# Kernel optimization log

Measured on AMD Instinct MI355X. Metric: run time of the kernel, lower is better.

The kernel has to match this reference:

```python
import jax, jax.numpy as jnp
import numpy as np
import math

DIM_MODEL = 1024
N_HEAD = 16
NUM_NEURON = 64
MAX_LEN = 2048
B, S = 4, 2048


def setup_inputs() -> dict:
    key = jax.random.key(0)
    ks = jax.random.split(key, 11)
    d, p = DIM_MODEL, N_HEAD * NUM_NEURON
    sc_in = 1.0 / math.sqrt(d)
    sc_p = 1.0 / math.sqrt(p)
    return {
        "q": jax.random.normal(ks[0], (B, S, d), jnp.float32),
        "k": jax.random.normal(ks[1], (B, S, d), jnp.float32),
        "v": jax.random.normal(ks[2], (B, S, d), jnp.float32),
        "Wq": jax.random.normal(ks[3], (d, p), jnp.float32) * sc_in,
        "bq": jnp.zeros((p,), jnp.float32),
        "Wk": jax.random.normal(ks[4], (d, p), jnp.float32) * sc_in,
        "bk": jnp.zeros((p,), jnp.float32),
        "Wv": jax.random.normal(ks[5], (d, p), jnp.float32) * sc_in,
        "bv": jnp.zeros((p,), jnp.float32),
        "Wf": jax.random.normal(ks[6], (p, d), jnp.float32) * sc_p,
        "bf": jnp.zeros((d,), jnp.float32),
    }


def _split_heads(x):  # [B,S,H*Dh] -> [B,H,S,Dh]
    b, s, _ = x.shape
    return x.reshape(b, s, N_HEAD, NUM_NEURON).transpose(0, 2, 1, 3)


def reference(q, k, v, Wq, bq, Wk, bk, Wv, bv, Wf, bf):
    qh = _split_heads(q @ Wq + bq)
    kh = _split_heads(k @ Wk + bk)
    vh = _split_heads(v @ Wv + bv)
    # NOTE: original scales by 1/sqrt(max_len), not 1/sqrt(head_dim)
    scores = jnp.einsum("bhqd,bhkd->bhqk", qh, kh) / math.sqrt(MAX_LEN)
    s = scores.shape[-1]
    causal = jnp.tril(jnp.ones((s, s), bool))  # [S,S]
    scores = jnp.where(causal[None, None], scores, -jnp.inf)
    attn = jax.nn.softmax(scores, axis=-1)
    out = jnp.einsum("bhqk,bhkd->bhqd", attn, vh)  # [B,H,S,Dh]
    c = out.transpose(0, 2, 1, 3).reshape(out.shape[0], out.shape[2], N_HEAD * NUM_NEURON)
    return c @ Wf + bf
```

## Files before the change

### kernel.cpp

```cpp
#include <hip/hip_runtime.h>
#include <stdint.h>

#define DMODEL 1024
#define NHEAD 16
#define DH 64
#define BB 4
#define SS 2048
#define MROWS (BB * SS)

typedef __bf16 bfx8 __attribute__((ext_vector_type(8)));
typedef float f32x4 __attribute__((ext_vector_type(4)));
typedef float fvec4 __attribute__((ext_vector_type(4)));
typedef int i32x4 __attribute__((ext_vector_type(4)));
typedef unsigned short u16x8 __attribute__((ext_vector_type(8)));
typedef unsigned short u16x4 __attribute__((ext_vector_type(4)));

__device__ __forceinline__ unsigned short f2bf(float f) {
    union { float f; unsigned int u; } v; v.f = f;
    unsigned int r = v.u + 0x7FFFu + ((v.u >> 16) & 1u);
    return (unsigned short)(r >> 16);
}

__device__ __forceinline__ unsigned int cvtpk(float lo, float hi) {
    unsigned int r;
    asm("v_cvt_pk_bf16_f32 %0, %1, %2" : "=v"(r) : "v"(lo), "v"(hi));
    return r;
}

typedef __attribute__((address_space(1))) const void gas_t;
typedef __attribute__((address_space(3))) void las_t;
__device__ __forceinline__ void gload_lds16(const void* g, void* l) {
    __builtin_amdgcn_global_load_lds((gas_t*)g, (las_t*)l, 16, 0, 0);
}

__device__ __forceinline__ int sigma_k(int i) {
    return (i & 0x20) | ((i & 0x0C) << 1) | ((i & 0x10) >> 2) | (i & 3);
}

__global__ void cvt3_kernel(const float* __restrict__ s0, const float* __restrict__ s1,
                            const float* __restrict__ s2,
                            unsigned short* __restrict__ d0, unsigned short* __restrict__ d1,
                            unsigned short* __restrict__ d2, int n8)
{
    const float* s = (blockIdx.y == 0) ? s0 : (blockIdx.y == 1) ? s1 : s2;
    unsigned short* d = (blockIdx.y == 0) ? d0 : (blockIdx.y == 1) ? d1 : d2;
    int i = blockIdx.x * blockDim.x + threadIdx.x;
    if (i >= n8) return;
    fvec4 a = *reinterpret_cast<const fvec4*>(&s[(size_t)i * 8]);
    fvec4 b = *reinterpret_cast<const fvec4*>(&s[(size_t)i * 8 + 4]);
    u16x8 o;
    #pragma unroll
    for (int j = 0; j < 4; ++j) { o[j] = f2bf(a[j]); o[j + 4] = f2bf(b[j]); }
    *reinterpret_cast<u16x8*>(&d[(size_t)i * 8]) = o;
}

__global__ void transpose_cvt3_kernel(const float* __restrict__ W0, unsigned short* __restrict__ T0,
                                      const float* __restrict__ W1, unsigned short* __restrict__ T1,
                                      const float* __restrict__ W2, unsigned short* __restrict__ T2)
{
    const float* W = (blockIdx.z == 0) ? W0 : (blockIdx.z == 1) ? W1 : W2;
    unsigned short* Wt = (blockIdx.z == 0) ? T0 : (blockIdx.z == 1) ? T1 : T2;
    __shared__ unsigned short t[64][72];
    const int tid = threadIdx.x;
    const int r0 = blockIdx.y * 64, c0 = blockIdx.x * 64;
    #pragma unroll
    for (int i = 0; i < 4; ++i) {
        int idx = tid + i * 256;
        int r = idx >> 4, c4 = idx & 15;
        fvec4 v = *reinterpret_cast<const fvec4*>(&W[(size_t)(r0 + r) * DMODEL + c0 + c4 * 4]);
        #pragma unroll
        for (int j = 0; j < 4; ++j) t[c4 * 4 + j][r] = f2bf(v[j]);
    }
    __syncthreads();
    #pragma unroll
    for (int i = 0; i < 2; ++i) {
        int idx = tid + i * 256;
        int r = idx >> 3, c8 = idx & 7;
        u16x8 v = *reinterpret_cast<const u16x8*>(&t[r][c8 * 8]);
        *reinterpret_cast<u16x8*>(&Wt[(size_t)(c0 + r) * DMODEL + r0 + c8 * 8]) = v;
    }
}

__global__ void transpose_v_kernel(const unsigned short* __restrict__ Vb,
                                   unsigned short* __restrict__ Vt)
{
    __shared__ unsigned short t[64][72];
    const int tid = threadIdx.x;
    const int s0 = blockIdx.x * 64, bh = blockIdx.y;
    const int b = bh >> 4, h = bh & 15;
    #pragma unroll
    for (int i = 0; i < 2; ++i) {
        int idx = tid + i * 256;
        int sr = idx >> 3, c8 = idx & 7;
        u16x8 v = *reinterpret_cast<const u16x8*>(
            &Vb[((size_t)b * SS + s0 + sr) * DMODEL + h * DH + c8 * 8]);
        #pragma unroll
        for (int j = 0; j < 8; ++j) t[c8 * 8 + j][sr] = v[j];
    }
    __syncthreads();
    #pragma unroll
    for (int i = 0; i < 2; ++i) {
        int idx = tid + i * 256;
        int dr = idx >> 3, s8 = idx & 7;
        u16x8 v = *reinterpret_cast<const u16x8*>(&t[dr][s8 * 8]);
        *reinterpret_cast<u16x8*>(&Vt[((size_t)bh * DH + dr) * SS + s0 + s8 * 8]) = v;
    }
}

struct GArg {
    const unsigned short* A;
    const unsigned short* Bt;
    const float* bias;
    void* O;
    float osc;
};

template<bool OUT_BF16>
__global__ __launch_bounds__(256, 2)
void gemm_kernel(GArg g0, GArg g1, int M, int N, int K)
{
    const GArg g = blockIdx.z ? g1 : g0;
    __shared__ unsigned short sA[128 * 64];
    __shared__ unsigned short sB[128 * 64];
    const int tid  = threadIdx.x;
    const int lane = tid & 63;
    const int wave = tid >> 6;
    const int wm = (wave >> 1) * 64, wn = (wave & 1) * 64;
    const int m0 = blockIdx.x * 128, n0 = blockIdx.y * 128;
    const int lr = lane & 15;
    const int lg = lane >> 4;

    f32x4 acc[4][4] = {};

    for (int kk0 = 0; kk0 < K; kk0 += 64) {
        __syncthreads();
        #pragma unroll
        for (int i = 0; i < 4; ++i) {
            int c = tid + i * 256;
            int row = c >> 3, col8 = c & 7;
            gload_lds16(&g.A[(size_t)(m0 + row) * K + kk0 + col8 * 8], &sA[c * 8]);
        }
        #pragma unroll
        for (int i = 0; i < 4; ++i) {
            int c = tid + i * 256;
            int row = c >> 3, col8 = c & 7;
            gload_lds16(&g.Bt[(size_t)(n0 + row) * K + kk0 + col8 * 8], &sB[c * 8]);
        }
        __syncthreads();

        bfx8 af[4][2], bfr[4][2];
        #pragma unroll
        for (int m = 0; m < 4; ++m)
            #pragma unroll
            for (int kk = 0; kk < 2; ++kk)
                af[m][kk] = *reinterpret_cast<const bfx8*>(
                    &sA[(wm + m * 16 + lr) * 64 + kk * 32 + lg * 8]);
        #pragma unroll
        for (int n = 0; n < 4; ++n)
            #pragma unroll
            for (int kk = 0; kk < 2; ++kk)
                bfr[n][kk] = *reinterpret_cast<const bfx8*>(
                    &sB[(wn + n * 16 + lr) * 64 + kk * 32 + lg * 8]);
        #pragma unroll
        for (int kk = 0; kk < 2; ++kk)
            #pragma unroll
            for (int m = 0; m < 4; ++m)
                #pragma unroll
                for (int n = 0; n < 4; ++n)
                    acc[m][n] = __builtin_amdgcn_mfma_f32_16x16x32_bf16(
                        af[m][kk], bfr[n][kk], acc[m][n], 0, 0, 0);
    }

    #pragma unroll
    for (int n = 0; n < 4; ++n) {
        int col = n0 + wn + n * 16 + lr;
        float bv = g.bias[col];
        #pragma unroll
        for (int m = 0; m < 4; ++m) {
            int rowb = m0 + wm + m * 16 + lg * 4;
            #pragma unroll
            for (int r = 0; r < 4; ++r) {
                float val = (acc[m][n][r] + bv) * g.osc;
                if (OUT_BF16)
                    ((unsigned short*)g.O)[(size_t)(rowb + r) * N + col] = f2bf(val);
                else
                    ((float*)g.O)[(size_t)(rowb + r) * N + col] = val;
            }
        }
    }
}

__global__ __launch_bounds__(256, 2)
void attn_kernel(const unsigned short* __restrict__ Q,
                 const unsigned short* __restrict__ K,
                 const unsigned short* __restrict__ Vt,
                 unsigned short* __restrict__ C)
{
    __shared__ unsigned short sK[64][72];
    __shared__ unsigned short sVt[64][72];

    const int tid  = threadIdx.x;
    const int lane = tid & 63;
    const int wave = tid >> 6;
    const int lr = lane & 15, lg = lane >> 4;
    const int bh = blockIdx.x;
    const int qt = (int)(gridDim.y - 1) - (int)blockIdx.y;
    const int b = bh >> 4, h = bh & 15;
    const int q0 = qt * 128;
    const size_t rowbase = (size_t)b * SS;
    const int hcol = h * DH;

    const int srow = tid >> 3, sc8 = tid & 7;
    const int sig0 = sigma_k(srow), sig1 = sigma_k(srow + 32);

    bfx8 aq[2][2];
    #pragma unroll
    for (int m = 0; m < 2; ++m) {
        int qr = q0 + wave * 32 + m * 16 + lr;
        const unsigned short* p = &Q[(rowbase + qr) * DMODEL + hcol + lg * 8];
        aq[m][0] = *reinterpret_cast<const bfx8*>(p);
        aq[m][1] = *reinterpret_cast<const bfx8*>(p + 32);
    }

    float m_run[2] = {0.f, 0.f};
    f32x4 l4[2] = {};
    f32x4 acc_o[2][4] = {};
    bool mz = true;
    const int qmax_wave = q0 + wave * 32 + 31;
    const int ntiles = 2 * qt + 2;

    for (int t = 0; t < ntiles; ++t) {
        const int k0 = t * 64;
        __syncthreads();
        *reinterpret_cast<u16x8*>(&sK[srow][sc8 * 8]) =
            *reinterpret_cast<const u16x8*>(
                &K[(rowbase + k0 + sig0) * DMODEL + hcol + sc8 * 8]);
        *reinterpret_cast<u16x8*>(&sK[srow + 32][sc8 * 8]) =
            *reinterpret_cast<const u16x8*>(
                &K[(rowbase + k0 + sig1) * DMODEL + hcol + sc8 * 8]);
        *reinterpret_cast<u16x8*>(&sVt[srow][sc8 * 8]) =
            *reinterpret_cast<const u16x8*>(
                &Vt[((size_t)bh * DH + srow) * SS + k0 + sc8 * 8]);
        *reinterpret_cast<u16x8*>(&sVt[srow + 32][sc8 * 8]) =
            *reinterpret_cast<const u16x8*>(
                &Vt[((size_t)bh * DH + srow + 32) * SS + k0 + sc8 * 8]);
        __syncthreads();
        if (k0 > qmax_wave) continue;

        f32x4 sc[2][4];
        #pragma unroll
        for (int nf = 0; nf < 4; ++nf) {
            bfx8 ak0 = *reinterpret_cast<const bfx8*>(&sK[nf * 16 + lr][lg * 8]);
            bfx8 ak1 = *reinterpret_cast<const bfx8*>(&sK[nf * 16 + lr][32 + lg * 8]);
            #pragma unroll
            for (int m = 0; m < 2; ++m) {
                f32x4 s = {0.f, 0.f, 0.f, 0.f};
                s = __builtin_amdgcn_mfma_f32_16x16x32_bf16(ak0, aq[m][0], s, 0, 0, 0);
                s = __builtin_amdgcn_mfma_f32_16x16x32_bf16(ak1, aq[m][1], s, 0, 0, 0);
                sc[m][nf] = s;
            }
        }
        #pragma unroll
        for (int m = 0; m < 2; ++m) {
            if (k0 + 63 > q0 + wave * 32 + m * 16) {
                int qrow = q0 + wave * 32 + m * 16 + lr;
                #pragma unroll
                for (int nf = 0; nf < 4; ++nf) {
                    int kb = k0 + ((nf >> 1) << 5) + (lg << 3) + ((nf & 1) << 2);
                    #pragma unroll
                    for (int r = 0; r < 4; ++r)
                        if (kb + r > qrow) sc[m][nf][r] = -3.0e38f;
                }
            }
        }
        f32x4 mx4 = sc[0][0];
        #pragma unroll
        for (int m = 0; m < 2; ++m)
            #pragma unroll
            for (int nf = 0; nf < 4; ++nf)
                #pragma unroll
                for (int r = 0; r < 4; ++r) mx4[r] = fmaxf(mx4[r], sc[m][nf][r]);
        float pmax = fmaxf(fmaxf(mx4[0], mx4[1]), fmaxf(mx4[2], mx4[3]));
        if (mz && __all(pmax <= 8.0f)) {
            #pragma unroll
            for (int m = 0; m < 2; ++m)
                #pragma unroll
                for (int nf = 0; nf < 4; ++nf) {
                    #pragma unroll
                    for (int r = 0; r < 4; ++r)
                        sc[m][nf][r] = __builtin_exp2f(sc[m][nf][r]);
                    l4[m] += sc[m][nf];
                }
        } else {
            mz = false;
            #pragma unroll
            for (int m = 0; m < 2; ++m) {
                float mx = fmaxf(fmaxf(mx4[0], mx4[1]), fmaxf(mx4[2], mx4[3]));
                mx = -3.0e38f;
                #pragma unroll
                for (int nf = 0; nf < 4; ++nf)
                    #pragma unroll
                    for (int r = 0; r < 4; ++r) mx = fmaxf(mx, sc[m][nf][r]);
                mx = fmaxf(mx, __shfl_xor(mx, 16, 64));
                mx = fmaxf(mx, __shfl_xor(mx, 32, 64));
                float mnew = fmaxf(m_run[m], mx);
                float fs = __builtin_exp2f(m_run[m] - mnew);
                m_run[m] = mnew;
                f32x4 ps = {0.f, 0.f, 0.f, 0.f};
                #pragma unroll
                for (int nf = 0; nf < 4; ++nf) {
                    #pragma unroll
                    for (int r = 0; r < 4; ++r)
                        sc[m][nf][r] = __builtin_exp2f(sc[m][nf][r] - mnew);
                    ps += sc[m][nf];
                }
                #pragma unroll
                for (int r = 0; r < 4; ++r) l4[m][r] = l4[m][r] * fs + ps[r];
                #pragma unroll
                for (int r = 0; r < 4; ++r) {
                    float fsa = __shfl(fs, lg * 4 + r, 64);
                    #pragma unroll
                    for (int d = 0; d < 4; ++d) acc_o[m][d][r] *= fsa;
                }
            }
        }
        #pragma unroll
        for (int h2 = 0; h2 < 2; ++h2) {
            union { i32x4 i; bfx8 b; } pa[2];
            #pragma unroll
            for (int m = 0; m < 2; ++m) {
                pa[m].i[0] = cvtpk(sc[m][2 * h2][0],     sc[m][2 * h2][1]);
                pa[m].i[1] = cvtpk(sc[m][2 * h2][2],     sc[m][2 * h2][3]);
                pa[m].i[2] = cvtpk(sc[m][2 * h2 + 1][0], sc[m][2 * h2 + 1][1]);
                pa[m].i[3] = cvtpk(sc[m][2 * h2 + 1][2], sc[m][2 * h2 + 1][3]);
            }
            #pragma unroll
            for (int d = 0; d < 4; ++d) {
                bfx8 bv = *reinterpret_cast<const bfx8*>(&sVt[d * 16 + lr][h2 * 32 + lg * 8]);
                acc_o[0][d] = __builtin_amdgcn_mfma_f32_16x16x32_bf16(pa[0].b, bv, acc_o[0][d], 0, 0, 0);
                acc_o[1][d] = __builtin_amdgcn_mfma_f32_16x16x32_bf16(pa[1].b, bv, acc_o[1][d], 0, 0, 0);
            }
        }
    }

    #pragma unroll
    for (int m = 0; m < 2; ++m) {
        float l = (l4[m][0] + l4[m][1]) + (l4[m][2] + l4[m][3]);
        l += __shfl_xor(l, 16, 64);
        l += __shfl_xor(l, 32, 64);
        float linv = 1.0f / l;
        float linva[4];
        #pragma unroll
        for (int r = 0; r < 4; ++r) linva[r] = __shfl(linv, lg * 4 + r, 64);
        const int qrb = q0 + wave * 32 + m * 16 + lg * 4;
        #pragma unroll
        for (int d = 0; d < 4; ++d) {
            int col = hcol + d * 16 + lr;
            #pragma unroll
            for (int r = 0; r < 4; ++r)
                C[(rowbase + qrb + r) * DMODEL + col] = f2bf(acc_o[m][d][r] * linva[r]);
        }
    }
}

extern "C" void kernel_launch(void* const* d_in, const int* in_sizes, int n_in,
                              void* d_out, int out_size, void* d_ws, size_t ws_size,
                              hipStream_t stream)
{
    const float* q  = (const float*)d_in[0];
    const float* k  = (const float*)d_in[1];
    const float* v  = (const float*)d_in[2];
    const float* Wq = (const float*)d_in[3];
    const float* bq = (const float*)d_in[4];
    const float* Wk = (const float*)d_in[5];
    const float* bk = (const float*)d_in[6];
    const float* Wv = (const float*)d_in[7];
    const float* bv = (const float*)d_in[8];
    const float* Wf = (const float*)d_in[9];
    const float* bf = (const float*)d_in[10];

    unsigned short* ws = (unsigned short*)d_ws;
    const size_t SZ = (size_t)MROWS * DMODEL;
    unsigned short* ws0 = ws;
    unsigned short* ws1 = ws + SZ;
    unsigned short* ws2 = ws + 2 * SZ;
    unsigned short* ws3 = ws + 3 * SZ;

    unsigned short* scr = (unsigned short*)d_out;
    unsigned short* WqT = scr;
    unsigned short* WkT = scr + 1048576;
    unsigned short* WvT = scr + 2097152;
    unsigned short* Qb  = scr + 4194304;

    const float qscale = 0.02209708691207961f * 1.44269504088896341f;

    const int n8 = (int)(SZ / 8);
    cvt3_kernel<<<dim3((n8 + 255) / 256, 3), 256, 0, stream>>>(q, k, v, ws0, ws1, ws2, n8);

    transpose_cvt3_kernel<<<dim3(16, 16, 3), 256, 0, stream>>>(Wq, WqT, Wk, WkT, Wv, WvT);

    dim3 gblk2(MROWS / 128, DMODEL / 128, 2);
    {
        GArg gq{ws0, WqT, bq, Qb,  qscale};
        GArg gk{ws1, WkT, bk, ws3, 1.0f};
        gemm_kernel<true><<<gblk2, 256, 0, stream>>>(gq, gk, MROWS, DMODEL, DMODEL);
    }
    dim3 gblk1(MROWS / 128, DMODEL / 128, 1);
    {
        GArg gv{ws2, WvT, bv, ws0, 1.0f};
        gemm_kernel<true><<<gblk1, 256, 0, stream>>>(gv, gv, MROWS, DMODEL, DMODEL);
    }
    transpose_v_kernel<<<dim3(SS / 64, BB * NHEAD), 256, 0, stream>>>(ws0, ws1);

    transpose_cvt3_kernel<<<dim3(16, 16, 1), 256, 0, stream>>>(Wf, ws0, Wf, ws0, Wf, ws0);

    attn_kernel<<<dim3(BB * NHEAD, SS / 128), 256, 0, stream>>>(Qb, ws3, ws1, ws2);

    {
        GArg gf{ws2, ws0, bf, (float*)d_out, 1.0f};
        gemm_kernel<false><<<gblk1, 256, 0, stream>>>(gf, gf, MROWS, DMODEL, DMODEL);
    }
}
```

Measured before the change: 214.9 us.

## Pre-tile K/V into swizzled blocks, double-buffer via direct LDS loads, pair causal q-tiles

New prep kernels repack K (row-permuted) and V (transposed) per head into contiguous 64x64 XOR-swizzled tiles. The attention kernel streams these tiles into a double-buffered LDS with global_load_lds so the next tile's load overlaps the current tile's compute, and each block handles a long and a short causal q-tile pair to balance work. Row sums are now computed by an MFMA against a vector of ones instead of scalar adds and shuffles. This adds extra prep-kernel passes and a full vmcnt wait plus barrier every tile, and the grid shrinks to 512 blocks.

Result: slower. 227.9 us (+6.0%).

```diff
diff --git a/kernel.cpp b/kernel.cpp
--- a/kernel.cpp
+++ b/kernel.cpp
@@ -31,6 +31,12 @@
 typedef __attribute__((address_space(3))) void las_t;
 __device__ __forceinline__ void gload_lds16(const void* g, void* l) {
     __builtin_amdgcn_global_load_lds((gas_t*)g, (las_t*)l, 16, 0, 0);
+}
+
+__device__ __forceinline__ void hard_barrier() {
+    __builtin_amdgcn_sched_barrier(0);
+    __builtin_amdgcn_s_barrier();
+    __builtin_amdgcn_sched_barrier(0);
 }
 
 __device__ __forceinline__ int sigma_k(int i) {
@@ -81,29 +87,48 @@
     }
 }
 
-__global__ void transpose_v_kernel(const unsigned short* __restrict__ Vb,
-                                   unsigned short* __restrict__ Vt)
+__global__ void kprep_kernel(const unsigned short* __restrict__ Kb,
+                             unsigned short* __restrict__ Kp)
+{
+    const int tid = threadIdx.x;
+    const int kt = blockIdx.x, bh = blockIdx.y;
+    const int b = bh >> 4, h = bh & 15;
+    const size_t tbase = ((size_t)bh * 32 + kt) * 4096;
+    #pragma unroll
+    for (int i = 0; i < 2; ++i) {
+        int idx = tid + i * 256;
+        int r = idx >> 3, c = idx & 7;
+        u16x8 v = *reinterpret_cast<const u16x8*>(
+            &Kb[((size_t)b * SS + kt * 64 + sigma_k(r)) * DMODEL + h * DH + c * 8]);
+        *reinterpret_cast<u16x8*>(&Kp[tbase + r * 64 + ((c ^ (r & 7)) * 8)]) = v;
+    }
+}
+
+__global__ void vprep_kernel(const unsigned short* __restrict__ Vb,
+                             unsigned short* __restrict__ Vp)
 {
     __shared__ unsigned short t[64][72];
     const int tid = threadIdx.x;
-    const int s0 = blockIdx.x * 64, bh = blockIdx.y;
+    const int kt = blockIdx.x, bh = blockIdx.y;
     const int b = bh >> 4, h = bh & 15;
     #pragma unroll
     for (int i = 0; i < 2; ++i) {
         int idx = tid + i * 256;
         int sr = idx >> 3, c8 = idx & 7;
         u16x8 v = *reinterpret_cast<const u16x8*>(
-            &Vb[((size_t)b * SS + s0 + sr) * DMODEL + h * DH + c8 * 8]);
+            &Vb[((size_t)b * SS + kt * 64 + sr) * DMODEL + h * DH + c8 * 8]);
         #pragma unroll
         for (int j = 0; j < 8; ++j) t[c8 * 8 + j][sr] = v[j];
     }
     __syncthreads();
+    const size_t tbase = ((size_t)bh * 32 + kt) * 4096;
     #pragma unroll
     for (int i = 0; i < 2; ++i) {
         int idx = tid + i * 256;
-        int dr = idx >> 3, s8 = idx & 7;
-        u16x8 v = *reinterpret_cast<const u16x8*>(&t[dr][s8 * 8]);
-        *reinterpret_cast<u16x8*>(&Vt[((size_t)bh * DH + dr) * SS + s0 + s8 * 8]) = v;
+        int dr = idx >> 3, p = idx & 7;
+        int srcc = p ^ (dr & 7);
+        u16x8 v = *reinterpret_cast<const u16x8*>(&t[dr][srcc * 8]);
+        *reinterpret_cast<u16x8*>(&Vp[tbase + dr * 64 + p * 8]) = v;
     }
 }
 
@@ -192,173 +217,182 @@
 
 __global__ __launch_bounds__(256, 2)
 void attn_kernel(const unsigned short* __restrict__ Q,
-                 const unsigned short* __restrict__ K,
-                 const unsigned short* __restrict__ Vt,
+                 const unsigned short* __restrict__ Kp,
+                 const unsigned short* __restrict__ Vp,
                  unsigned short* __restrict__ C)
 {
-    __shared__ unsigned short sK[64][72];
-    __shared__ unsigned short sVt[64][72];
+    __shared__ unsigned short lds[2][8192];
 
     const int tid  = threadIdx.x;
     const int lane = tid & 63;
     const int wave = tid >> 6;
     const int lr = lane & 15, lg = lane >> 4;
-    const int bh = blockIdx.x;
-    const int qt = (int)(gridDim.y - 1) - (int)blockIdx.y;
+    const int pr = blockIdx.x;
+    const int bh = blockIdx.y;
     const int b = bh >> 4, h = bh & 15;
-    const int q0 = qt * 128;
     const size_t rowbase = (size_t)b * SS;
     const int hcol = h * DH;
-
-    const int srow = tid >> 3, sc8 = tid & 7;
-    const int sig0 = sigma_k(srow), sig1 = sigma_k(srow + 32);
-
-    bfx8 aq[2][2];
-    #pragma unroll
-    for (int m = 0; m < 2; ++m) {
-        int qr = q0 + wave * 32 + m * 16 + lr;
-        const unsigned short* p = &Q[(rowbase + qr) * DMODEL + hcol + lg * 8];
-        aq[m][0] = *reinterpret_cast<const bfx8*>(p);
-        aq[m][1] = *reinterpret_cast<const bfx8*>(p + 32);
-    }
-
-    float m_run[2] = {0.f, 0.f};
-    f32x4 l4[2] = {};
-    f32x4 acc_o[2][4] = {};
-    bool mz = true;
-    const int qmax_wave = q0 + wave * 32 + 31;
-    const int ntiles = 2 * qt + 2;
-
-    for (int t = 0; t < ntiles; ++t) {
-        const int k0 = t * 64;
-        __syncthreads();
-        *reinterpret_cast<u16x8*>(&sK[srow][sc8 * 8]) =
-            *reinterpret_cast<const u16x8*>(
-                &K[(rowbase + k0 + sig0) * DMODEL + hcol + sc8 * 8]);
-        *reinterpret_cast<u16x8*>(&sK[srow + 32][sc8 * 8]) =
-            *reinterpret_cast<const u16x8*>(
-                &K[(rowbase + k0 + sig1) * DMODEL + hcol + sc8 * 8]);
-        *reinterpret_cast<u16x8*>(&sVt[srow][sc8 * 8]) =
-            *reinterpret_cast<const u16x8*>(
-                &Vt[((size_t)bh * DH + srow) * SS + k0 + sc8 * 8]);
-        *reinterpret_cast<u16x8*>(&sVt[srow + 32][sc8 * 8]) =
-            *reinterpret_cast<const u16x8*>(
-                &Vt[((size_t)bh * DH + srow + 32) * SS + k0 + sc8 * 8]);
-        __syncthreads();
-        if (k0 > qmax_wave) continue;
-
-        f32x4 sc[2][4];
-        #pragma unroll
-        for (int nf = 0; nf < 4; ++nf) {
-            bfx8 ak0 = *reinterpret_cast<const bfx8*>(&sK[nf * 16 + lr][lg * 8]);
-            bfx8 ak1 = *reinterpret_cast<const bfx8*>(&sK[nf * 16 + lr][32 + lg * 8]);
-            #pragma unroll
-            for (int m = 0; m < 2; ++m) {
-                f32x4 s = {0.f, 0.f, 0.f, 0.f};
-                s = __builtin_amdgcn_mfma_f32_16x16x32_bf16(ak0, aq[m][0], s, 0, 0, 0);
-                s = __builtin_amdgcn_mfma_f32_16x16x32_bf16(ak1, aq[m][1], s, 0, 0, 0);
-                sc[m][nf] = s;
+    const int p0 = lg ^ (lr & 7);
+
+    const u16x8 onesu = {0x3F80, 0x3F80, 0x3F80, 0x3F80, 0x3F80, 0x3F80, 0x3F80, 0x3F80};
+    union { u16x8 u; bfx8 b; } onesc; onesc.u = onesu;
+    const bfx8 ones = onesc.b;
+
+    #pragma unroll
+    for (int ph = 0; ph < 2; ++ph) {
+        const int qt = ph ? pr : (15 - pr);
+        const int q0 = qt * 128;
+
+        bfx8 aq[2][2];
+        #pragma unroll
+        for (int m = 0; m < 2; ++m) {
+            int qr = q0 + wave * 32 + m * 16 + lr;
+            const unsigned short* p = &Q[(rowbase + qr) * DMODEL + hcol + lg * 8];
+            aq[m][0] = *reinterpret_cast<const bfx8*>(p);
+            aq[m][1] = *reinterpret_cast<const bfx8*>(p + 32);
+        }
+
+        float m_run[2] = {0.f, 0.f};
+        f32x4 acc_l[2] = {};
+        f32x4 acc_o[2][4] = {};
+        bool mz = true;
+        const int qmax_wave = q0 + wave * 32 + 31;
+        const int ntiles = 2 * qt + 2;
+
+        {
+            const size_t tb = ((size_t)bh * 32 + 0) * 4096;
+            gload_lds16(&Kp[tb + (size_t)tid * 8],         &lds[0][tid * 8]);
+            gload_lds16(&Kp[tb + (size_t)(tid + 256) * 8], &lds[0][(tid + 256) * 8]);
+            gload_lds16(&Vp[tb + (size_t)tid * 8],         &lds[0][4096 + tid * 8]);
+            gload_lds16(&Vp[tb + (size_t)(tid + 256) * 8], &lds[0][4096 + (tid + 256) * 8]);
+        }
+        asm volatile("s_waitcnt vmcnt(0)" ::: "memory");
+        hard_barrier();
+
+        for (int t = 0; t < ntiles; ++t) {
+            const int cur = t & 1;
+            if (t + 1 < ntiles) {
+                const size_t tb = ((size_t)bh * 32 + t + 1) * 4096;
+                gload_lds16(&Kp[tb + (size_t)tid * 8],         &lds[cur ^ 1][tid * 8]);
+                gload_lds16(&Kp[tb + (size_t)(tid + 256) * 8], &lds[cur ^ 1][(tid + 256) * 8]);
+                gload_lds16(&Vp[tb + (size_t)tid * 8],         &lds[cur ^ 1][4096 + tid * 8]);
+                gload_lds16(&Vp[tb + (size_t)(tid + 256) * 8], &lds[cur ^ 1][4096 + (tid + 256) * 8]);
             }
-        }
-        #pragma unroll
-        for (int m = 0; m < 2; ++m) {
-            if (k0 + 63 > q0 + wave * 32 + m * 16) {
-                int qrow = q0 + wave * 32 + m * 16 + lr;
+            const int k0 = t * 64;
+            if (k0 <= qmax_wave) {
+                const unsigned short* kb = &lds[cur][0];
+                const unsigned short* vb = &lds[cur][4096];
+                f32x4 sc[2][4];
                 #pragma unroll
                 for (int nf = 0; nf < 4; ++nf) {
-                    int kb = k0 + ((nf >> 1) << 5) + (lg << 3) + ((nf & 1) << 2);
-                    #pragma unroll
-                    for (int r = 0; r < 4; ++r)
-                        if (kb + r > qrow) sc[m][nf][r] = -3.0e38f;
+                    int i = nf * 16 + lr;
+                    bfx8 ak0 = *reinterpret_cast<const bfx8*>(&kb[i * 64 + p0 * 8]);
+                    bfx8 ak1 = *reinterpret_cast<const bfx8*>(&kb[i * 64 + (p0 ^ 4) * 8]);
+                    #pragma unroll
+                    for (int m = 0; m < 2; ++m) {
+                        f32x4 s = {0.f, 0.f, 0.f, 0.f};
+                        s = __builtin_amdgcn_mfma_f32_16x16x32_bf16(ak0, aq[m][0], s, 0, 0, 0);
+                        s = __builtin_amdgcn_mfma_f32_16x16x32_bf16(ak1, aq[m][1], s, 0, 0, 0);
+                        sc[m][nf] = s;
+                    }
+                }
+                #pragma unroll
+                for (int m = 0; m < 2; ++m) {
+                    if (k0 + 63 > q0 + wave * 32 + m * 16) {
+                        int qrow = q0 + wave * 32 + m * 16 + lr;
+                        #pragma unroll
+                        for (int nf = 0; nf < 4; ++nf) {
+                            int kb_ = k0 + ((nf >> 1) << 5) + (lg << 3) + ((nf & 1) << 2);
+                            #pragma unroll
+                            for (int r = 0; r < 4; ++r)
+                                if (kb_ + r > qrow) sc[m][nf][r] = -3.0e38f;
+                        }
+                    }
+                }
+                float pmax = -3.0e38f;
+                #pragma unroll
+                for (int m = 0; m < 2; ++m)
+                    #pragma unroll
+                    for (int nf = 0; nf < 4; ++nf) {
+                        float a = fmaxf(fmaxf(sc[m][nf][0], sc[m][nf][1]),
+                                        fmaxf(sc[m][nf][2], sc[m][nf][3]));
+                        pmax = fmaxf(pmax, a);
+                    }
+                if (mz && __all(pmax <= 8.0f)) {
+                    #pragma unroll
+                    for (int m = 0; m < 2; ++m)
+                        #pragma unroll
+                        for (int nf = 0; nf < 4; ++nf)
+                            #pragma unroll
+                            for (int r = 0; r < 4; ++r)
+                                sc[m][nf][r] = __builtin_exp2f(sc[m][nf][r]);
+                } else {
+                    mz = false;
+                    #pragma unroll
+                    for (int m = 0; m < 2; ++m) {
+                        float mx = -3.0e38f;
+                        #pragma unroll
+                        for (int nf = 0; nf < 4; ++nf)
+                            #pragma unroll
+                            for (int r = 0; r < 4; ++r) mx = fmaxf(mx, sc[m][nf][r]);
+                        mx = fmaxf(mx, __shfl_xor(mx, 16, 64));
+                        mx = fmaxf(mx, __shfl_xor(mx, 32, 64));
+                        float mnew = fmaxf(m_run[m], mx);
+                        float fs = __builtin_exp2f(m_run[m] - mnew);
+                        m_run[m] = mnew;
+                        #pragma unroll
+                        for (int nf = 0; nf < 4; ++nf)
+                            #pragma unroll
+                            for (int r = 0; r < 4; ++r)
+                                sc[m][nf][r] = __builtin_exp2f(sc[m][nf][r] - mnew);
+                        #pragma unroll
+                        for (int r = 0; r < 4; ++r) {
+                            float fsa = __shfl(fs, lg * 4 + r, 64);
+                            #pragma unroll
+                            for (int d = 0; d < 4; ++d) acc_o[m][d][r] *= fsa;
+                            acc_l[m][r] *= fsa;
+                        }
+                    }
+                }
+                #pragma unroll
+                for (int h2 = 0; h2 < 2; ++h2) {
+                    union { i32x4 i; bfx8 b; } pa[2];
+                    #pragma unroll
+                    for (int m = 0; m < 2; ++m) {
+                        pa[m].i[0] = cvtpk(sc[m][2 * h2][0],     sc[m][2 * h2][1]);
+                        pa[m].i[1] = cvtpk(sc[m][2 * h2][2],     sc[m][2 * h2][3]);
+                        pa[m].i[2] = cvtpk(sc[m][2 * h2 + 1][0], sc[m][2 * h2 + 1][1]);
+                        pa[m].i[3] = cvtpk(sc[m][2 * h2 + 1][2], sc[m][2 * h2 + 1][3]);
+                    }
+                    acc_l[0] = __builtin_amdgcn_mfma_f32_16x16x32_bf16(pa[0].b, ones, acc_l[0], 0, 0, 0);
+                    acc_l[1] = __builtin_amdgcn_mfma_f32_16x16x32_bf16(pa[1].b, ones, acc_l[1], 0, 0, 0);
+                    #pragma unroll
+                    for (int d = 0; d < 4; ++d) {
+                        int dd = d * 16 + lr;
+                        int pv = ((h2 << 2) | lg) ^ (lr & 7);
+                        bfx8 bv = *reinterpret_cast<const bfx8*>(&vb[dd * 64 + pv * 8]);
+                        acc_o[0][d] = __builtin_amdgcn_mfma_f32_16x16x32_bf16(pa[0].b, bv, acc_o[0][d], 0, 0, 0);
+                        acc_o[1][d] = __builtin_amdgcn_mfma_f32_16x16x32_bf16(pa[1].b, bv, acc_o[1][d], 0, 0, 0);
+                    }
                 }
             }
-        }
-        f32x4 mx4 = sc[0][0];
-        #pragma unroll
-        for (int m = 0; m < 2; ++m)
-            #pragma unroll
-            for (int nf = 0; nf < 4; ++nf)
-                #pragma unroll
-                for (int r = 0; r < 4; ++r) mx4[r] = fmaxf(mx4[r], sc[m][nf][r]);
-        float pmax = fmaxf(fmaxf(mx4[0], mx4[1]), fmaxf(mx4[2], mx4[3]));
-        if (mz && __all(pmax <= 8.0f)) {
-            #pragma unroll
-            for (int m = 0; m < 2; ++m)
-                #pragma unroll
-                for (int nf = 0; nf < 4; ++nf) {
-                    #pragma unroll
-                    for (int r = 0; r < 4; ++r)
-                        sc[m][nf][r] = __builtin_exp2f(sc[m][nf][r]);
-                    l4[m] += sc[m][nf];
-                }
-        } else {
-            mz = false;
-            #pragma unroll
-            for (int m = 0; m < 2; ++m) {
-                float mx = fmaxf(fmaxf(mx4[0], mx4[1]), fmaxf(mx4[2], mx4[3]));
-                mx = -3.0e38f;
-                #pragma unroll
-                for (int nf = 0; nf < 4; ++nf)
-                    #pragma unroll
-                    for (int r = 0; r < 4; ++r) mx = fmaxf(mx, sc[m][nf][r]);
-                mx = fmaxf(mx, __shfl_xor(mx, 16, 64));
-                mx = fmaxf(mx, __shfl_xor(mx, 32, 64));
-                float mnew = fmaxf(m_run[m], mx);
-                float fs = __builtin_exp2f(m_run[m] - mnew);
-                m_run[m] = mnew;
-                f32x4 ps = {0.f, 0.f, 0.f, 0.f};
-                #pragma unroll
-                for (int nf = 0; nf < 4; ++nf) {
-                    #pragma unroll
-                    for (int r = 0; r < 4; ++r)
-                        sc[m][nf][r] = __builtin_exp2f(sc[m][nf][r] - mnew);
-                    ps += sc[m][nf];
-                }
-                #pragma unroll
-                for (int r = 0; r < 4; ++r) l4[m][r] = l4[m][r] * fs + ps[r];
-                #pragma unroll
-                for (int r = 0; r < 4; ++r) {
-                    float fsa = __shfl(fs, lg * 4 + r, 64);
-                    #pragma unroll
-                    for (int d = 0; d < 4; ++d) acc_o[m][d][r] *= fsa;
-                }
+            asm volatile("s_waitcnt vmcnt(0)" ::: "memory");
+            hard_barrier();
+        }
+
+        #pragma unroll
+        for (int m = 0; m < 2; ++m) {
+            const int qrb = q0 + wave * 32 + m * 16 + lg * 4;
+            f32x4 linv;
+            #pragma unroll
+            for (int r = 0; r < 4; ++r) linv[r] = 1.0f / acc_l[m][r];
+            #pragma unroll
+            for (int d = 0; d < 4; ++d) {
+                int col = hcol + d * 16 + lr;
+                #pragma unroll
+                for (int r = 0; r < 4; ++r)
+                    C[(rowbase + qrb + r) * DMODEL + col] = f2bf(acc_o[m][d][r] * linv[r]);
             }
-        }
-        #pragma unroll
-        for (int h2 = 0; h2 < 2; ++h2) {
-            union { i32x4 i; bfx8 b; } pa[2];
-            #pragma unroll
-            for (int m = 0; m < 2; ++m) {
-                pa[m].i[0] = cvtpk(sc[m][2 * h2][0],     sc[m][2 * h2][1]);
-                pa[m].i[1] = cvtpk(sc[m][2 * h2][2],     sc[m][2 * h2][3]);
-                pa[m].i[2] = cvtpk(sc[m][2 * h2 + 1][0], sc[m][2 * h2 + 1][1]);
-                pa[m].i[3] = cvtpk(sc[m][2 * h2 + 1][2], sc[m][2 * h2 + 1][3]);
-            }
-            #pragma unroll
-            for (int d = 0; d < 4; ++d) {
-                bfx8 bv = *reinterpret_cast<const bfx8*>(&sVt[d * 16 + lr][h2 * 32 + lg * 8]);
-                acc_o[0][d] = __builtin_amdgcn_mfma_f32_16x16x32_bf16(pa[0].b, bv, acc_o[0][d], 0, 0, 0);
-                acc_o[1][d] = __builtin_amdgcn_mfma_f32_16x16x32_bf16(pa[1].b, bv, acc_o[1][d], 0, 0, 0);
-            }
-        }
-    }
-
-    #pragma unroll
-    for (int m = 0; m < 2; ++m) {
-        float l = (l4[m][0] + l4[m][1]) + (l4[m][2] + l4[m][3]);
-        l += __shfl_xor(l, 16, 64);
-        l += __shfl_xor(l, 32, 64);
-        float linv = 1.0f / l;
-        float linva[4];
-        #pragma unroll
-        for (int r = 0; r < 4; ++r) linva[r] = __shfl(linv, lg * 4 + r, 64);
-        const int qrb = q0 + wave * 32 + m * 16 + lg * 4;
-        #pragma unroll
-        for (int d = 0; d < 4; ++d) {
-            int col = hcol + d * 16 + lr;
-            #pragma unroll
-            for (int r = 0; r < 4; ++r)
-                C[(rowbase + qrb + r) * DMODEL + col] = f2bf(acc_o[m][d][r] * linva[r]);
         }
     }
 }
@@ -410,14 +444,12 @@
         GArg gv{ws2, WvT, bv, ws0, 1.0f};
         gemm_kernel<true><<<gblk1, 256, 0, stream>>>(gv, gv, MROWS, DMODEL, DMODEL);
     }
-    transpose_v_kernel<<<dim3(SS / 64, BB * NHEAD), 256, 0, stream>>>(ws0, ws1);
-
-    transpose_cvt3_kernel<<<dim3(16, 16, 1), 256, 0, stream>>>(Wf, ws0, Wf, ws0, Wf, ws0);
-
-    attn_kernel<<<dim3(BB * NHEAD, SS / 128), 256, 0, stream>>>(Qb, ws3, ws1, ws2);
-
+    kprep_kernel<<<dim3(SS / 64, BB * NHEAD), 256, 0, stream>>>(ws3, ws1);
+    vprep_kernel<<<dim3(SS / 64, BB * NHEAD), 256, 0, stream>>>(ws0, ws2);
+    transpose_cvt3_kernel<<<dim3(16, 16, 1), 256, 0, stream>>>(Wf, ws3, Wf, ws3, Wf, ws3);
+    attn_kernel<<<dim3(8, BB * NHEAD), 256, 0, stream>>>(Qb, ws1, ws2, ws0);
     {
-        GArg gf{ws2, ws0, bf, (float*)d_out, 1.0f};
+        GArg gf{ws0, ws3, bf, (float*)d_out, 1.0f};
         gemm_kernel<false><<<gblk1, 256, 0, stream>>>(gf, gf, MROWS, DMODEL, DMODEL);
     }
 }
```

## Fuse V transpose into V-projection GEMM epilogue and add MFMA priority hints

Applied to the files above, without the earlier changes.

The V projection GEMM now writes its bf16 output directly in the per-head transposed [B,H,Dh,S] layout that attention consumes, using packed 4-element stores. This removes the separate transpose_v kernel launch and one full round trip of V through global memory. The GEMM output type becomes a runtime mode instead of a template parameter, and workspace buffers are reassigned to match. The attention kernel also raises wave priority with s_setprio around its MFMA blocks, aiming to interleave matrix and softmax work better across waves.

Result: no change. 212.8 us (-1.0%).

```diff
diff --git a/kernel.cpp b/kernel.cpp
--- a/kernel.cpp
+++ b/kernel.cpp
@@ -81,41 +81,15 @@
     }
 }
 
-__global__ void transpose_v_kernel(const unsigned short* __restrict__ Vb,
-                                   unsigned short* __restrict__ Vt)
-{
-    __shared__ unsigned short t[64][72];
-    const int tid = threadIdx.x;
-    const int s0 = blockIdx.x * 64, bh = blockIdx.y;
-    const int b = bh >> 4, h = bh & 15;
-    #pragma unroll
-    for (int i = 0; i < 2; ++i) {
-        int idx = tid + i * 256;
-        int sr = idx >> 3, c8 = idx & 7;
-        u16x8 v = *reinterpret_cast<const u16x8*>(
-            &Vb[((size_t)b * SS + s0 + sr) * DMODEL + h * DH + c8 * 8]);
-        #pragma unroll
-        for (int j = 0; j < 8; ++j) t[c8 * 8 + j][sr] = v[j];
-    }
-    __syncthreads();
-    #pragma unroll
-    for (int i = 0; i < 2; ++i) {
-        int idx = tid + i * 256;
-        int dr = idx >> 3, s8 = idx & 7;
-        u16x8 v = *reinterpret_cast<const u16x8*>(&t[dr][s8 * 8]);
-        *reinterpret_cast<u16x8*>(&Vt[((size_t)bh * DH + dr) * SS + s0 + s8 * 8]) = v;
-    }
-}
-
 struct GArg {
     const unsigned short* A;
     const unsigned short* Bt;
     const float* bias;
     void* O;
     float osc;
+    int mode;
 };
 
-template<bool OUT_BF16>
 __global__ __launch_bounds__(256, 2)
 void gemm_kernel(GArg g0, GArg g1, int M, int N, int K)
 {
@@ -178,13 +152,25 @@
         #pragma unroll
         for (int m = 0; m < 4; ++m) {
             int rowb = m0 + wm + m * 16 + lg * 4;
-            #pragma unroll
-            for (int r = 0; r < 4; ++r) {
-                float val = (acc[m][n][r] + bv) * g.osc;
-                if (OUT_BF16)
-                    ((unsigned short*)g.O)[(size_t)(rowb + r) * N + col] = f2bf(val);
-                else
-                    ((float*)g.O)[(size_t)(rowb + r) * N + col] = val;
+            float val[4];
+            #pragma unroll
+            for (int r = 0; r < 4; ++r) val[r] = (acc[m][n][r] + bv) * g.osc;
+            if (g.mode == 0) {
+                #pragma unroll
+                for (int r = 0; r < 4; ++r)
+                    ((unsigned short*)g.O)[(size_t)(rowb + r) * N + col] = f2bf(val[r]);
+            } else if (g.mode == 2) {
+                #pragma unroll
+                for (int r = 0; r < 4; ++r)
+                    ((float*)g.O)[(size_t)(rowb + r) * N + col] = val[r];
+            } else {
+                int bq = rowb >> 11, s = rowb & 2047;
+                int hh = col >> 6, d = col & 63;
+                u16x4 pk;
+                #pragma unroll
+                for (int r = 0; r < 4; ++r) pk[r] = f2bf(val[r]);
+                size_t idx = ((size_t)(bq * 16 + hh) * 64 + d) * 2048 + s;
+                *reinterpret_cast<u16x4*>(&((unsigned short*)g.O)[idx]) = pk;
             }
         }
     }
@@ -248,6 +234,7 @@
         if (k0 > qmax_wave) continue;
 
         f32x4 sc[2][4];
+        __builtin_amdgcn_s_setprio(1);
         #pragma unroll
         for (int nf = 0; nf < 4; ++nf) {
             bfx8 ak0 = *reinterpret_cast<const bfx8*>(&sK[nf * 16 + lr][lg * 8]);
@@ -260,6 +247,7 @@
                 sc[m][nf] = s;
             }
         }
+        __builtin_amdgcn_s_setprio(0);
         #pragma unroll
         for (int m = 0; m < 2; ++m) {
             if (k0 + 63 > q0 + wave * 32 + m * 16) {
@@ -295,8 +283,7 @@
             mz = false;
             #pragma unroll
             for (int m = 0; m < 2; ++m) {
-                float mx = fmaxf(fmaxf(mx4[0], mx4[1]), fmaxf(mx4[2], mx4[3]));
-                mx = -3.0e38f;
+                float mx = -3.0e38f;
                 #pragma unroll
                 for (int nf = 0; nf < 4; ++nf)
                     #pragma unroll
@@ -334,12 +321,14 @@
                 pa[m].i[2] = cvtpk(sc[m][2 * h2 + 1][0], sc[m][2 * h2 + 1][1]);
                 pa[m].i[3] = cvtpk(sc[m][2 * h2 + 1][2], sc[m][2 * h2 + 1][3]);
             }
+            __builtin_amdgcn_s_setprio(1);
             #pragma unroll
             for (int d = 0; d < 4; ++d) {
-                bfx8 bv = *reinterpret_cast<const bfx8*>(&sVt[d * 16 + lr][h2 * 32 + lg * 8]);
-                acc_o[0][d] = __builtin_amdgcn_mfma_f32_16x16x32_bf16(pa[0].b, bv, acc_o[0][d], 0, 0, 0);
-                acc_o[1][d] = __builtin_amdgcn_mfma_f32_16x16x32_bf16(pa[1].b, bv, acc_o[1][d], 0, 0, 0);
-            }
+                bfx8 bv0 = *reinterpret_cast<const bfx8*>(&sVt[d * 16 + lr][h2 * 32 + lg * 8]);
+                acc_o[0][d] = __builtin_amdgcn_mfma_f32_16x16x32_bf16(pa[0].b, bv0, acc_o[0][d], 0, 0, 0);
+                acc_o[1][d] = __builtin_amdgcn_mfma_f32_16x16x32_bf16(pa[1].b, bv0, acc_o[1][d], 0, 0, 0);
+            }
+            __builtin_amdgcn_s_setprio(0);
         }
     }
 
@@ -399,25 +388,21 @@
 
     transpose_cvt3_kernel<<<dim3(16, 16, 3), 256, 0, stream>>>(Wq, WqT, Wk, WkT, Wv, WvT);
 
-    dim3 gblk2(MROWS / 128, DMODEL / 128, 2);
     {
-        GArg gq{ws0, WqT, bq, Qb,  qscale};
-        GArg gk{ws1, WkT, bk, ws3, 1.0f};
-        gemm_kernel<true><<<gblk2, 256, 0, stream>>>(gq, gk, MROWS, DMODEL, DMODEL);
-    }
-    dim3 gblk1(MROWS / 128, DMODEL / 128, 1);
+        GArg gq{ws0, WqT, bq, Qb,  qscale, 0};
+        GArg gk{ws1, WkT, bk, ws3, 1.0f,   0};
+        gemm_kernel<<<dim3(64, 8, 2), 256, 0, stream>>>(gq, gk, MROWS, DMODEL, DMODEL);
+    }
     {
-        GArg gv{ws2, WvT, bv, ws0, 1.0f};
-        gemm_kernel<true><<<gblk1, 256, 0, stream>>>(gv, gv, MROWS, DMODEL, DMODEL);
-    }
-    transpose_v_kernel<<<dim3(SS / 64, BB * NHEAD), 256, 0, stream>>>(ws0, ws1);
-
-    transpose_cvt3_kernel<<<dim3(16, 16, 1), 256, 0, stream>>>(Wf, ws0, Wf, ws0, Wf, ws0);
-
-    attn_kernel<<<dim3(BB * NHEAD, SS / 128), 256, 0, stream>>>(Qb, ws3, ws1, ws2);
+        GArg gv{ws2, WvT, bv, ws0, 1.0f, 3};
+        gemm_kernel<<<dim3(64, 8, 1), 256, 0, stream>>>(gv, gv, MROWS, DMODEL, DMODEL);
+    }
+    transpose_cvt3_kernel<<<dim3(16, 16, 1), 256, 0, stream>>>(Wf, ws2, Wf, ws2, Wf, ws2);
+
+    attn_kernel<<<dim3(BB * NHEAD, SS / 128), 256, 0, stream>>>(Qb, ws3, ws0, ws1);
 
     {
-        GArg gf{ws2, ws0, bf, (float*)d_out, 1.0f};
-        gemm_kernel<false><<<gblk1, 256, 0, stream>>>(gf, gf, MROWS, DMODEL, DMODEL);
-    }
-}
+        GArg gf{ws1, ws2, bf, (float*)d_out, 1.0f, 2};
+        gemm_kernel<<<dim3(64, 8, 1), 256, 0, stream>>>(gf, gf, MROWS, DMODEL, DMODEL);
+    }
+}
```
